# Performance work log

Hardware: AMD Instinct MI355X
Metric: run time of the kernel (lower is better)

Reference implementation:

```python
import jax, jax.numpy as jnp
import numpy as np

D = 128
N_NODES = 50000
N_EDGES = 500000


def layer_norm(x, g, b, eps=1e-5):
    m = jnp.mean(x, axis=-1, keepdims=True)
    v = jnp.var(x, axis=-1, keepdims=True)
    return (x - m) * jax.lax.rsqrt(v + eps) * g + b


def setup_inputs() -> dict:
    key = jax.random.key(0)
    ks = jax.random.split(key, 10)
    s = 1.0 / np.sqrt(D)  # torch Linear default-ish init scale
    return {
        "src": jax.random.normal(ks[0], (N_NODES, D), jnp.float32),
        "tgt": jax.random.normal(ks[1], (N_NODES, D), jnp.float32),
        "edge": jax.random.normal(ks[2], (N_EDGES, D), jnp.float32),
        "src_idx": jax.random.randint(ks[3], (N_EDGES,), 0, N_NODES, jnp.int64 if jax.config.jax_enable_x64 else jnp.int32),
        "tgt_idx": jax.random.randint(ks[4], (N_EDGES,), 0, N_NODES, jnp.int64 if jax.config.jax_enable_x64 else jnp.int32),
        "W_s2e": jax.random.normal(ks[5], (D, D), jnp.float32) * s,
        "W_t2e": jax.random.normal(ks[6], (D, D), jnp.float32) * s,
        "W_e2e": jax.random.normal(ks[7], (D, D), jnp.float32) * s,
        "W_e2t": jax.random.normal(ks[8], (D, D), jnp.float32) * s,
        "W_t2t": jax.random.normal(ks[9], (D, D), jnp.float32) * s,
        "ln1_g": jnp.ones((D,), jnp.float32),
        "ln1_b": jnp.zeros((D,), jnp.float32),
        "ln2_g": jnp.ones((D,), jnp.float32),
        "ln2_b": jnp.zeros((D,), jnp.float32),
    }


def reference(src, tgt, edge, src_idx, tgt_idx,
              W_s2e, W_t2e, W_e2e, W_e2t, W_t2t,
              ln1_g, ln1_b, ln2_g, ln2_b):
    # ---- STE2E: source/target/edge -> edge update ----
    # gather endpoint node features per edge [E, D]
    msg = (src[src_idx] @ W_s2e.T
           + tgt[tgt_idx] @ W_t2e.T
           + edge @ W_e2e.T)
    edge_out = edge + layer_norm(jax.nn.silu(msg), ln1_g, ln1_b)

    # ---- ET2T: aggregate edges to target nodes, update targets ----
    agg = jax.ops.segment_sum(edge_out, tgt_idx, num_segments=tgt.shape[0])  # [N, D]
    tgt_msg = agg @ W_e2t.T + tgt @ W_t2t.T
    tgt_out = tgt + layer_norm(jax.nn.silu(tgt_msg), ln2_g, ln2_b)

    return edge_out, tgt_out
```

## Files before the change

### kernel.cpp

```cpp
#include <hip/hip_runtime.h>
#include <hip/hip_bf16.h>

#define D 128
#define LDSPAD 136

typedef short s8v __attribute__((ext_vector_type(8)));
typedef float f4v __attribute__((ext_vector_type(4)));

__device__ inline short f2bf(float f) {
    __hip_bfloat16 h = __float2bfloat16(f);
    return *reinterpret_cast<short*>(&h);
}

__device__ inline void load_w_lds(const float* __restrict__ W, short* lds) {
    const int tid = threadIdx.x;
    const float4* W4 = reinterpret_cast<const float4*>(W);
#pragma unroll
    for (int i = 0; i < 16; ++i) {
        int f = tid + 256 * i;
        float4 v = W4[f];
        int row = f >> 5;
        int c4  = (f & 31) * 4;
        short* p = &lds[row * LDSPAD + c4];
        p[0] = f2bf(v.x); p[1] = f2bf(v.y);
        p[2] = f2bf(v.z); p[3] = f2bf(v.w);
    }
}

__device__ inline void mfma_tile(const float* __restrict__ X, int row0,
                                 const short* lds, f4v acc[8]) {
    const int lane = threadIdx.x & 63;
    const int l15 = lane & 15, q = lane >> 4;
    s8v a[4];
    const float* xr = X + (size_t)(row0 + l15) * D + q * 8;
#pragma unroll
    for (int c = 0; c < 4; ++c) {
        float4 f0 = *reinterpret_cast<const float4*>(xr + c * 32);
        float4 f1 = *reinterpret_cast<const float4*>(xr + c * 32 + 4);
        s8v t;
        t[0] = f2bf(f0.x); t[1] = f2bf(f0.y); t[2] = f2bf(f0.z); t[3] = f2bf(f0.w);
        t[4] = f2bf(f1.x); t[5] = f2bf(f1.y); t[6] = f2bf(f1.z); t[7] = f2bf(f1.w);
        a[c] = t;
    }
#pragma unroll
    for (int t = 0; t < 8; ++t) {
        f4v acc_t = {0.f, 0.f, 0.f, 0.f};
#pragma unroll
        for (int c = 0; c < 4; ++c) {
            const s8v b = *reinterpret_cast<const s8v*>(
                &lds[(t * 16 + l15) * LDSPAD + c * 32 + q * 8]);
            acc_t = __builtin_amdgcn_mfma_f32_16x16x32_bf16(a[c], b, acc_t, 0, 0, 0);
        }
        acc[t] = acc_t;
    }
}


__global__ __launch_bounds__(256) void k_zero_i(int* p, int n) {
    int i = blockIdx.x * 256 + threadIdx.x;
    if (i < n) p[i] = 0;
}

__global__ __launch_bounds__(256) void k_hist(const int* __restrict__ tidx,
                                              int* __restrict__ cnt, int E) {
    int i = blockIdx.x * 256 + threadIdx.x;
    if (i < E) atomicAdd(&cnt[tidx[i]], 1);
}

__global__ __launch_bounds__(1024) void k_scan(const int* __restrict__ cnt,
                                               int* __restrict__ off,
                                               int* __restrict__ cursor, int n) {
    __shared__ int part[1024];
    const int tid = threadIdx.x;
    const int chunk = (n + 1023) / 1024;
    const int lo = tid * chunk;
    const int hi = min(lo + chunk, n);
    int s = 0;
    for (int i = lo; i < hi; ++i) s += cnt[i];
    part[tid] = s;
    __syncthreads();
    for (int d = 1; d < 1024; d <<= 1) {
        int v = (tid >= d) ? part[tid - d] : 0;
        __syncthreads();
        part[tid] += v;
        __syncthreads();
    }
    int run = part[tid] - s;
    for (int i = lo; i < hi; ++i) {
        off[i] = run;
        cursor[i] = run;
        run += cnt[i];
    }
    if (tid == 0) off[n] = part[1023];
}

__global__ __launch_bounds__(256) void k_scatter(const int* __restrict__ tidx,
                                                 int* __restrict__ cursor,
                                                 int* __restrict__ elist, int E) {
    int i = blockIdx.x * 256 + threadIdx.x;
    if (i < E) {
        int p = atomicAdd(&cursor[tidx[i]], 1);
        elist[p] = i;
    }
}


__global__ __launch_bounds__(256) void k_node_gemm(const float* __restrict__ X,
                                                   const float* __restrict__ W,
                                                   float* __restrict__ P, int nrows) {
    __shared__ short lds[D * LDSPAD];
    load_w_lds(W, lds);
    __syncthreads();
    const int lane = threadIdx.x & 63, wave = threadIdx.x >> 6;
    const int l15 = lane & 15, q = lane >> 4;
    const int ntiles = nrows >> 4;
    for (int tile = blockIdx.x * 4 + wave; tile < ntiles; tile += gridDim.x * 4) {
        f4v acc[8];
        mfma_tile(X, tile * 16, lds, acc);
#pragma unroll
        for (int t = 0; t < 8; ++t) {
            int col = t * 16 + l15;
#pragma unroll
            for (int r = 0; r < 4; ++r)
                P[(size_t)(tile * 16 + q * 4 + r) * D + col] = acc[t][r];
        }
    }
}

__global__ __launch_bounds__(256) void k_edge(const float* __restrict__ edge,
                                              const int* __restrict__ sidx,
                                              const int* __restrict__ tidx,
                                              const float* __restrict__ W,
                                              const float* __restrict__ Ps,
                                              const float* __restrict__ Pt,
                                              const float* __restrict__ g1,
                                              const float* __restrict__ b1,
                                              float* __restrict__ eout, int E) {
    __shared__ short lds[D * LDSPAD];
    load_w_lds(W, lds);
    __syncthreads();
    const int lane = threadIdx.x & 63, wave = threadIdx.x >> 6;
    const int l15 = lane & 15, q = lane >> 4;
    const int ntiles = E >> 4;
    for (int tile = blockIdx.x * 4 + wave; tile < ntiles; tile += gridDim.x * 4) {
        const int e0 = tile * 16;
        f4v acc[8];
        mfma_tile(edge, e0, lds, acc);
        int si[4], ti[4];
#pragma unroll
        for (int r = 0; r < 4; ++r) {
            si[r] = sidx[e0 + q * 4 + r];
            ti[r] = tidx[e0 + q * 4 + r];
        }
        float h[8][4];
        float s1[4] = {0.f, 0.f, 0.f, 0.f}, s2[4] = {0.f, 0.f, 0.f, 0.f};
#pragma unroll
        for (int t = 0; t < 8; ++t) {
            int col = t * 16 + l15;
#pragma unroll
            for (int r = 0; r < 4; ++r) {
                float m = acc[t][r] + Ps[(size_t)si[r] * D + col]
                                    + Pt[(size_t)ti[r] * D + col];
                float hh = m / (1.f + __expf(-m));
                h[t][r] = hh;
                s1[r] += hh;
                s2[r] += hh * hh;
            }
        }
#pragma unroll
        for (int m = 1; m < 16; m <<= 1) {
#pragma unroll
            for (int r = 0; r < 4; ++r) {
                s1[r] += __shfl_xor(s1[r], m, 64);
                s2[r] += __shfl_xor(s2[r], m, 64);
            }
        }
        float mean[4], rstd[4];
#pragma unroll
        for (int r = 0; r < 4; ++r) {
            float mu = s1[r] * (1.f / 128.f);
            float var = s2[r] * (1.f / 128.f) - mu * mu;
            mean[r] = mu;
            rstd[r] = rsqrtf(var + 1e-5f);
        }
#pragma unroll
        for (int t = 0; t < 8; ++t) {
            int col = t * 16 + l15;
            float gg = g1[col], bb = b1[col];
#pragma unroll
            for (int r = 0; r < 4; ++r) {
                int rowg = e0 + q * 4 + r;
                float v = edge[(size_t)rowg * D + col]
                          + ((h[t][r] - mean[r]) * rstd[r] * gg + bb);
                eout[(size_t)rowg * D + col] = v;
            }
        }
    }
}

__global__ __launch_bounds__(256) void k_agg(const float* __restrict__ eout,
                                             const int* __restrict__ off,
                                             const int* __restrict__ elist,
                                             float* __restrict__ agg, int N) {
    const int node = blockIdx.x * 4 + (threadIdx.x >> 6);
    const int lane = threadIdx.x & 63;
    if (node >= N) return;
    const int lo = off[node], hi = off[node + 1];
    float ax = 0.f, ay = 0.f;
    for (int j = lo; j < hi; ++j) {
        int e = elist[j];
        float2 v = *reinterpret_cast<const float2*>(&eout[(size_t)e * D + 2 * lane]);
        ax += v.x; ay += v.y;
    }
    float2 o = {ax, ay};
    *reinterpret_cast<float2*>(&agg[(size_t)node * D + 2 * lane]) = o;
}

__global__ __launch_bounds__(256) void k_node_update(const float* __restrict__ aggIn,
                                                     const float* __restrict__ W,
                                                     const float* __restrict__ Ptt,
                                                     const float* __restrict__ tgt,
                                                     const float* __restrict__ g2,
                                                     const float* __restrict__ b2,
                                                     float* __restrict__ out, int N) {
    __shared__ short lds[D * LDSPAD];
    load_w_lds(W, lds);
    __syncthreads();
    const int lane = threadIdx.x & 63, wave = threadIdx.x >> 6;
    const int l15 = lane & 15, q = lane >> 4;
    const int ntiles = N >> 4;
    for (int tile = blockIdx.x * 4 + wave; tile < ntiles; tile += gridDim.x * 4) {
        const int n0 = tile * 16;
        f4v acc[8];
        mfma_tile(aggIn, n0, lds, acc);
        float h[8][4];
        float s1[4] = {0.f, 0.f, 0.f, 0.f}, s2[4] = {0.f, 0.f, 0.f, 0.f};
#pragma unroll
        for (int t = 0; t < 8; ++t) {
            int col = t * 16 + l15;
#pragma unroll
            for (int r = 0; r < 4; ++r) {
                int rowg = n0 + q * 4 + r;
                float m = acc[t][r] + Ptt[(size_t)rowg * D + col];
                float hh = m / (1.f + __expf(-m));
                h[t][r] = hh;
                s1[r] += hh;
                s2[r] += hh * hh;
            }
        }
#pragma unroll
        for (int m = 1; m < 16; m <<= 1) {
#pragma unroll
            for (int r = 0; r < 4; ++r) {
                s1[r] += __shfl_xor(s1[r], m, 64);
                s2[r] += __shfl_xor(s2[r], m, 64);
            }
        }
        float mean[4], rstd[4];
#pragma unroll
        for (int r = 0; r < 4; ++r) {
            float mu = s1[r] * (1.f / 128.f);
            float var = s2[r] * (1.f / 128.f) - mu * mu;
            mean[r] = mu;
            rstd[r] = rsqrtf(var + 1e-5f);
        }
#pragma unroll
        for (int t = 0; t < 8; ++t) {
            int col = t * 16 + l15;
            float gg = g2[col], bb = b2[col];
#pragma unroll
            for (int r = 0; r < 4; ++r) {
                int rowg = n0 + q * 4 + r;
                float v = tgt[(size_t)rowg * D + col]
                          + ((h[t][r] - mean[r]) * rstd[r] * gg + bb);
                out[(size_t)rowg * D + col] = v;
            }
        }
    }
}

extern "C" void kernel_launch(void* const* d_in, const int* in_sizes, int n_in,
                              void* d_out, int out_size, void* d_ws, size_t ws_size,
                              hipStream_t stream) {
    const float* src   = (const float*)d_in[0];
    const float* tgt   = (const float*)d_in[1];
    const float* edge  = (const float*)d_in[2];
    const int*   sidx  = (const int*)d_in[3];
    const int*   tidx  = (const int*)d_in[4];
    const float* W_s2e = (const float*)d_in[5];
    const float* W_t2e = (const float*)d_in[6];
    const float* W_e2e = (const float*)d_in[7];
    const float* W_e2t = (const float*)d_in[8];
    const float* W_t2t = (const float*)d_in[9];
    const float* g1    = (const float*)d_in[10];
    const float* b1    = (const float*)d_in[11];
    const float* g2    = (const float*)d_in[12];
    const float* b2    = (const float*)d_in[13];

    const int N = in_sizes[0] / D;
    const int E = in_sizes[3];

    float* eout = (float*)d_out;
    float* nout = eout + (size_t)E * D;

    float* Ps  = (float*)d_ws;
    float* Pt  = Ps + (size_t)N * D;
    float* Ptt = Pt + (size_t)N * D;
    int*   cnt    = (int*)(Ptt + (size_t)N * D);
    int*   off    = cnt + N;
    int*   cursor = off + N + 1;
    int*   elist  = cursor + N;

    k_zero_i<<<(N + 255) / 256, 256, 0, stream>>>(cnt, N);
    k_hist<<<(E + 255) / 256, 256, 0, stream>>>(tidx, cnt, E);
    k_scan<<<1, 1024, 0, stream>>>(cnt, off, cursor, N);
    k_scatter<<<(E + 255) / 256, 256, 0, stream>>>(tidx, cursor, elist, E);

    const int nodeBlocks = (N / 16 + 3) / 4;
    k_node_gemm<<<nodeBlocks, 256, 0, stream>>>(src, W_s2e, Ps, N);
    k_node_gemm<<<nodeBlocks, 256, 0, stream>>>(tgt, W_t2e, Pt, N);
    k_node_gemm<<<nodeBlocks, 256, 0, stream>>>(tgt, W_t2t, Ptt, N);

    k_edge<<<1024, 256, 0, stream>>>(edge, sidx, tidx, W_e2e, Ps, Pt, g1, b1,
                                     eout, E);

    k_agg<<<(N + 3) / 4, 256, 0, stream>>>(eout, off, elist, nout, N);
    k_node_update<<<nodeBlocks, 256, 0, stream>>>(nout, W_e2t, Ptt, tgt, g2, b2,
                                                  nout, N);
}
```

Before: 914.5 us.

## Preconvert weights to bf16 once, fuse tgt GEMMs, drop LDS in node kernels

A new prep kernel converts all five weight matrices to bf16 in workspace and also zeroes the histogram counts, replacing the separate zero kernel. The two GEMMs that read tgt are fused into one kernel so the A tile is built once. Node kernels now use one tile per wave and read B straight from global or L2 instead of staging it in LDS, and they declare occupancy hints. The edge kernel copies the pre-converted bf16 weights into LDS, uses a reciprocal-based SiLU, and is split into two launches over halves of the edges. These changes aim to cut repeated fp32-to-bf16 conversion, weight staging and extra reads of tgt, at the cost of more global B traffic and one extra launch.

```diff
diff --git a/kernel.cpp b/kernel.cpp
--- a/kernel.cpp
+++ b/kernel.cpp
@@ -5,6 +5,7 @@
 #define LDSPAD 136
 
 typedef short s8v __attribute__((ext_vector_type(8)));
+typedef short s4v __attribute__((ext_vector_type(4)));
 typedef float f4v __attribute__((ext_vector_type(4)));
 
 __device__ inline short f2bf(float f) {
@@ -12,26 +13,50 @@
     return *reinterpret_cast<short*>(&h);
 }
 
-__device__ inline void load_w_lds(const float* __restrict__ W, short* lds) {
+__device__ inline float fast_silu(float m) {
+    return m * __builtin_amdgcn_rcpf(1.f + __expf(-m));
+}
+
+__global__ __launch_bounds__(256) void k_prep(const float* __restrict__ W0,
+                                              const float* __restrict__ W1,
+                                              const float* __restrict__ W2,
+                                              const float* __restrict__ W3,
+                                              const float* __restrict__ W4,
+                                              short* __restrict__ Wbf,
+                                              int* __restrict__ cnt, int N) {
+    const int b = blockIdx.x, tid = threadIdx.x;
+    if (b < 80) {
+        int g = b * 256 + tid;
+        int m = g >> 12;
+        const float* W = W0;
+        if (m == 1) W = W1; else if (m == 2) W = W2;
+        else if (m == 3) W = W3; else if (m == 4) W = W4;
+        int w = g & 4095;
+        float4 v = reinterpret_cast<const float4*>(W)[w];
+        s4v o;
+        o[0] = f2bf(v.x); o[1] = f2bf(v.y); o[2] = f2bf(v.z); o[3] = f2bf(v.w);
+        *reinterpret_cast<s4v*>(&Wbf[(size_t)m * 16384 + w * 4]) = o;
+    } else {
+        int i = (b - 80) * 256 + tid;
+        if (i < N) cnt[i] = 0;
+    }
+}
+
+__device__ inline void load_wbf_lds(const short* __restrict__ Wb, short* lds) {
     const int tid = threadIdx.x;
-    const float4* W4 = reinterpret_cast<const float4*>(W);
-#pragma unroll
-    for (int i = 0; i < 16; ++i) {
+    const int4* src = reinterpret_cast<const int4*>(Wb);
+#pragma unroll
+    for (int i = 0; i < 8; ++i) {
         int f = tid + 256 * i;
-        float4 v = W4[f];
-        int row = f >> 5;
-        int c4  = (f & 31) * 4;
-        short* p = &lds[row * LDSPAD + c4];
-        p[0] = f2bf(v.x); p[1] = f2bf(v.y);
-        p[2] = f2bf(v.z); p[3] = f2bf(v.w);
-    }
-}
-
-__device__ inline void mfma_tile(const float* __restrict__ X, int row0,
-                                 const short* lds, f4v acc[8]) {
+        int4 v = src[f];
+        int row = f >> 4, c = f & 15;
+        *reinterpret_cast<int4*>(&lds[row * LDSPAD + c * 8]) = v;
+    }
+}
+
+__device__ inline void build_a(const float* __restrict__ X, int row0, s8v a[4]) {
     const int lane = threadIdx.x & 63;
     const int l15 = lane & 15, q = lane >> 4;
-    s8v a[4];
     const float* xr = X + (size_t)(row0 + l15) * D + q * 8;
 #pragma unroll
     for (int c = 0; c < 4; ++c) {
@@ -42,6 +67,11 @@
         t[4] = f2bf(f1.x); t[5] = f2bf(f1.y); t[6] = f2bf(f1.z); t[7] = f2bf(f1.w);
         a[c] = t;
     }
+}
+
+__device__ inline void mfma_b_lds(const s8v a[4], const short* lds, f4v acc[8]) {
+    const int lane = threadIdx.x & 63;
+    const int l15 = lane & 15, q = lane >> 4;
 #pragma unroll
     for (int t = 0; t < 8; ++t) {
         f4v acc_t = {0.f, 0.f, 0.f, 0.f};
@@ -55,11 +85,23 @@
     }
 }
 
-
-__global__ __launch_bounds__(256) void k_zero_i(int* p, int n) {
-    int i = blockIdx.x * 256 + threadIdx.x;
-    if (i < n) p[i] = 0;
-}
+__device__ inline void mfma_b_g(const s8v a[4], const short* __restrict__ Wb,
+                                f4v acc[8]) {
+    const int lane = threadIdx.x & 63;
+    const int l15 = lane & 15, q = lane >> 4;
+#pragma unroll
+    for (int t = 0; t < 8; ++t) {
+        f4v acc_t = {0.f, 0.f, 0.f, 0.f};
+#pragma unroll
+        for (int c = 0; c < 4; ++c) {
+            const s8v b = *reinterpret_cast<const s8v*>(
+                &Wb[(t * 16 + l15) * D + c * 32 + q * 8]);
+            acc_t = __builtin_amdgcn_mfma_f32_16x16x32_bf16(a[c], b, acc_t, 0, 0, 0);
+        }
+        acc[t] = acc_t;
+    }
+}
+
 
 __global__ __launch_bounds__(256) void k_hist(const int* __restrict__ tidx,
                                               int* __restrict__ cnt, int E) {
@@ -105,54 +147,80 @@
 }
 
 
-__global__ __launch_bounds__(256) void k_node_gemm(const float* __restrict__ X,
-                                                   const float* __restrict__ W,
-                                                   float* __restrict__ P, int nrows) {
+__global__ __launch_bounds__(256, 4) void k_gemm1(const float* __restrict__ X,
+                                                  const short* __restrict__ Wb,
+                                                  float* __restrict__ P, int ntiles) {
+    const int lane = threadIdx.x & 63, wave = threadIdx.x >> 6;
+    const int l15 = lane & 15, q = lane >> 4;
+    const int tile = blockIdx.x * 4 + wave;
+    if (tile >= ntiles) return;
+    s8v a[4];
+    build_a(X, tile * 16, a);
+    f4v acc[8];
+    mfma_b_g(a, Wb, acc);
+#pragma unroll
+    for (int t = 0; t < 8; ++t) {
+        int col = t * 16 + l15;
+#pragma unroll
+        for (int r = 0; r < 4; ++r)
+            P[(size_t)(tile * 16 + q * 4 + r) * D + col] = acc[t][r];
+    }
+}
+
+__global__ __launch_bounds__(256, 4) void k_gemm2(const float* __restrict__ X,
+                                                  const short* __restrict__ Wb1,
+                                                  const short* __restrict__ Wb2,
+                                                  float* __restrict__ P1,
+                                                  float* __restrict__ P2, int ntiles) {
+    const int lane = threadIdx.x & 63, wave = threadIdx.x >> 6;
+    const int l15 = lane & 15, q = lane >> 4;
+    const int tile = blockIdx.x * 4 + wave;
+    if (tile >= ntiles) return;
+    s8v a[4];
+    build_a(X, tile * 16, a);
+    f4v acc1[8], acc2[8];
+    mfma_b_g(a, Wb1, acc1);
+    mfma_b_g(a, Wb2, acc2);
+#pragma unroll
+    for (int t = 0; t < 8; ++t) {
+        int col = t * 16 + l15;
+#pragma unroll
+        for (int r = 0; r < 4; ++r) {
+            size_t o = (size_t)(tile * 16 + q * 4 + r) * D + col;
+            P1[o] = acc1[t][r];
+            P2[o] = acc2[t][r];
+        }
+    }
+}
+
+__global__ __launch_bounds__(256, 4) void k_edge(const float* __restrict__ edge,
+                                                 const int* __restrict__ sidx,
+                                                 const int* __restrict__ tidx,
+                                                 const short* __restrict__ Wb,
+                                                 const float* __restrict__ Ps,
+                                                 const float* __restrict__ Pt,
+                                                 const float* __restrict__ g1,
+                                                 const float* __restrict__ b1,
+                                                 float* __restrict__ eout,
+                                                 int tile0, int tile1) {
     __shared__ short lds[D * LDSPAD];
-    load_w_lds(W, lds);
+    load_wbf_lds(Wb, lds);
     __syncthreads();
     const int lane = threadIdx.x & 63, wave = threadIdx.x >> 6;
     const int l15 = lane & 15, q = lane >> 4;
-    const int ntiles = nrows >> 4;
-    for (int tile = blockIdx.x * 4 + wave; tile < ntiles; tile += gridDim.x * 4) {
-        f4v acc[8];
-        mfma_tile(X, tile * 16, lds, acc);
-#pragma unroll
-        for (int t = 0; t < 8; ++t) {
-            int col = t * 16 + l15;
-#pragma unroll
-            for (int r = 0; r < 4; ++r)
-                P[(size_t)(tile * 16 + q * 4 + r) * D + col] = acc[t][r];
-        }
-    }
-}
-
-__global__ __launch_bounds__(256) void k_edge(const float* __restrict__ edge,
-                                              const int* __restrict__ sidx,
-                                              const int* __restrict__ tidx,
-                                              const float* __restrict__ W,
-                                              const float* __restrict__ Ps,
-                                              const float* __restrict__ Pt,
-                                              const float* __restrict__ g1,
-                                              const float* __restrict__ b1,
-                                              float* __restrict__ eout, int E) {
-    __shared__ short lds[D * LDSPAD];
-    load_w_lds(W, lds);
-    __syncthreads();
-    const int lane = threadIdx.x & 63, wave = threadIdx.x >> 6;
-    const int l15 = lane & 15, q = lane >> 4;
-    const int ntiles = E >> 4;
-    for (int tile = blockIdx.x * 4 + wave; tile < ntiles; tile += gridDim.x * 4) {
+    for (int tile = tile0 + blockIdx.x * 4 + wave; tile < tile1;
+         tile += gridDim.x * 4) {
         const int e0 = tile * 16;
-        f4v acc[8];
-        mfma_tile(edge, e0, lds, acc);
         int si[4], ti[4];
 #pragma unroll
         for (int r = 0; r < 4; ++r) {
             si[r] = sidx[e0 + q * 4 + r];
             ti[r] = tidx[e0 + q * 4 + r];
         }
-        float h[8][4];
+        s8v a[4];
+        build_a(edge, e0, a);
+        f4v acc[8];
+        mfma_b_lds(a, lds, acc);
         float s1[4] = {0.f, 0.f, 0.f, 0.f}, s2[4] = {0.f, 0.f, 0.f, 0.f};
 #pragma unroll
         for (int t = 0; t < 8; ++t) {
@@ -161,8 +229,8 @@
             for (int r = 0; r < 4; ++r) {
                 float m = acc[t][r] + Ps[(size_t)si[r] * D + col]
                                     + Pt[(size_t)ti[r] * D + col];
-                float hh = m / (1.f + __expf(-m));
-                h[t][r] = hh;
+                float hh = fast_silu(m);
+                acc[t][r] = hh;
                 s1[r] += hh;
                 s2[r] += hh * hh;
             }
@@ -191,7 +259,7 @@
             for (int r = 0; r < 4; ++r) {
                 int rowg = e0 + q * 4 + r;
                 float v = edge[(size_t)rowg * D + col]
-                          + ((h[t][r] - mean[r]) * rstd[r] * gg + bb);
+                          + ((acc[t][r] - mean[r]) * rstd[r] * gg + bb);
                 eout[(size_t)rowg * D + col] = v;
             }
         }
@@ -216,65 +284,62 @@
     *reinterpret_cast<float2*>(&agg[(size_t)node * D + 2 * lane]) = o;
 }
 
-__global__ __launch_bounds__(256) void k_node_update(const float* __restrict__ aggIn,
-                                                     const float* __restrict__ W,
-                                                     const float* __restrict__ Ptt,
-                                                     const float* __restrict__ tgt,
-                                                     const float* __restrict__ g2,
-                                                     const float* __restrict__ b2,
-                                                     float* __restrict__ out, int N) {
-    __shared__ short lds[D * LDSPAD];
-    load_w_lds(W, lds);
-    __syncthreads();
+__global__ __launch_bounds__(256, 4) void k_node_update(const float* __restrict__ aggIn,
+                                                        const short* __restrict__ Wb,
+                                                        const float* __restrict__ Ptt,
+                                                        const float* __restrict__ tgt,
+                                                        const float* __restrict__ g2,
+                                                        const float* __restrict__ b2,
+                                                        float* __restrict__ out, int ntiles) {
     const int lane = threadIdx.x & 63, wave = threadIdx.x >> 6;
     const int l15 = lane & 15, q = lane >> 4;
-    const int ntiles = N >> 4;
-    for (int tile = blockIdx.x * 4 + wave; tile < ntiles; tile += gridDim.x * 4) {
-        const int n0 = tile * 16;
-        f4v acc[8];
-        mfma_tile(aggIn, n0, lds, acc);
-        float h[8][4];
-        float s1[4] = {0.f, 0.f, 0.f, 0.f}, s2[4] = {0.f, 0.f, 0.f, 0.f};
-#pragma unroll
-        for (int t = 0; t < 8; ++t) {
-            int col = t * 16 + l15;
-#pragma unroll
-            for (int r = 0; r < 4; ++r) {
-                int rowg = n0 + q * 4 + r;
-                float m = acc[t][r] + Ptt[(size_t)rowg * D + col];
-                float hh = m / (1.f + __expf(-m));
-                h[t][r] = hh;
-                s1[r] += hh;
-                s2[r] += hh * hh;
-            }
-        }
-#pragma unroll
-        for (int m = 1; m < 16; m <<= 1) {
-#pragma unroll
-            for (int r = 0; r < 4; ++r) {
-                s1[r] += __shfl_xor(s1[r], m, 64);
-                s2[r] += __shfl_xor(s2[r], m, 64);
-            }
-        }
-        float mean[4], rstd[4];
-#pragma unroll
-        for (int r = 0; r < 4; ++r) {
-            float mu = s1[r] * (1.f / 128.f);
-            float var = s2[r] * (1.f / 128.f) - mu * mu;
-            mean[r] = mu;
-            rstd[r] = rsqrtf(var + 1e-5f);
-        }
-#pragma unroll
-        for (int t = 0; t < 8; ++t) {
-            int col = t * 16 + l15;
-            float gg = g2[col], bb = b2[col];
-#pragma unroll
-            for (int r = 0; r < 4; ++r) {
-                int rowg = n0 + q * 4 + r;
-                float v = tgt[(size_t)rowg * D + col]
-                          + ((h[t][r] - mean[r]) * rstd[r] * gg + bb);
-                out[(size_t)rowg * D + col] = v;
-            }
+    const int tile = blockIdx.x * 4 + wave;
+    if (tile >= ntiles) return;
+    const int n0 = tile * 16;
+    s8v a[4];
+    build_a(aggIn, n0, a);
+    f4v acc[8];
+    mfma_b_g(a, Wb, acc);
+    float s1[4] = {0.f, 0.f, 0.f, 0.f}, s2[4] = {0.f, 0.f, 0.f, 0.f};
+#pragma unroll
+    for (int t = 0; t < 8; ++t) {
+        int col = t * 16 + l15;
+#pragma unroll
+        for (int r = 0; r < 4; ++r) {
+            int rowg = n0 + q * 4 + r;
+            float m = acc[t][r] + Ptt[(size_t)rowg * D + col];
+            float hh = fast_silu(m);
+            acc[t][r] = hh;
+            s1[r] += hh;
+            s2[r] += hh * hh;
+        }
+    }
+#pragma unroll
+    for (int m = 1; m < 16; m <<= 1) {
+#pragma unroll
+        for (int r = 0; r < 4; ++r) {
+            s1[r] += __shfl_xor(s1[r], m, 64);
+            s2[r] += __shfl_xor(s2[r], m, 64);
+        }
+    }
+    float mean[4], rstd[4];
+#pragma unroll
+    for (int r = 0; r < 4; ++r) {
+        float mu = s1[r] * (1.f / 128.f);
+        float var = s2[r] * (1.f / 128.f) - mu * mu;
+        mean[r] = mu;
+        rstd[r] = rsqrtf(var + 1e-5f);
+    }
+#pragma unroll
+    for (int t = 0; t < 8; ++t) {
+        int col = t * 16 + l15;
+        float gg = g2[col], bb = b2[col];
+#pragma unroll
+        for (int r = 0; r < 4; ++r) {
+            int rowg = n0 + q * 4 + r;
+            float v = tgt[(size_t)rowg * D + col]
+                      + ((acc[t][r] - mean[r]) * rstd[r] * gg + bb);
+            out[(size_t)rowg * D + col] = v;
         }
     }
 }
@@ -303,7 +368,8 @@
     float* eout = (float*)d_out;
     float* nout = eout + (size_t)E * D;
 
-    float* Ps  = (float*)d_ws;
+    short* Wbf = (short*)d_ws;
+    float* Ps  = (float*)(Wbf + 5 * 16384);
     float* Pt  = Ps + (size_t)N * D;
     float* Ptt = Pt + (size_t)N * D;
     int*   cnt    = (int*)(Ptt + (size_t)N * D);
@@ -311,20 +377,33 @@
     int*   cursor = off + N + 1;
     int*   elist  = cursor + N;
 
-    k_zero_i<<<(N + 255) / 256, 256, 0, stream>>>(cnt, N);
+    const short* Wb_s2e = Wbf;
+    const short* Wb_t2e = Wbf + 1 * 16384;
+    const short* Wb_e2e = Wbf + 2 * 16384;
+    const short* Wb_e2t = Wbf + 3 * 16384;
+    const short* Wb_t2t = Wbf + 4 * 16384;
+
+    const int zeroBlocks = (N + 255) / 256;
+    k_prep<<<80 + zeroBlocks, 256, 0, stream>>>(W_s2e, W_t2e, W_e2e, W_e2t, W_t2t,
+                                                Wbf, cnt, N);
+
     k_hist<<<(E + 255) / 256, 256, 0, stream>>>(tidx, cnt, E);
     k_scan<<<1, 1024, 0, stream>>>(cnt, off, cursor, N);
     k_scatter<<<(E + 255) / 256, 256, 0, stream>>>(tidx, cursor, elist, E);
 
-    const int nodeBlocks = (N / 16 + 3) / 4;
-    k_node_gemm<<<nodeBlocks, 256, 0, stream>>>(src, W_s2e, Ps, N);
-    k_node_gemm<<<nodeBlocks, 256, 0, stream>>>(tgt, W_t2e, Pt, N);
-    k_node_gemm<<<nodeBlocks, 256, 0, stream>>>(tgt, W_t2t, Ptt, N);
-
-    k_edge<<<1024, 256, 0, stream>>>(edge, sidx, tidx, W_e2e, Ps, Pt, g1, b1,
-                                     eout, E);
+    const int ntilesN = N >> 4;
+    const int nodeBlocks = (ntilesN + 3) / 4;
+    k_gemm1<<<nodeBlocks, 256, 0, stream>>>(src, Wb_s2e, Ps, ntilesN);
+    k_gemm2<<<nodeBlocks, 256, 0, stream>>>(tgt, Wb_t2e, Wb_t2t, Pt, Ptt, ntilesN);
+
+    const int ntilesE = E >> 4;
+    const int halfE = ntilesE >> 1;
+    k_edge<<<1024, 256, 0, stream>>>(edge, sidx, tidx, Wb_e2e, Ps, Pt, g1, b1,
+                                     eout, 0, halfE);
+    k_edge<<<1024, 256, 0, stream>>>(edge, sidx, tidx, Wb_e2e, Ps, Pt, g1, b1,
+                                     eout, halfE, ntilesE);
 
     k_agg<<<(N + 3) / 4, 256, 0, stream>>>(eout, off, elist, nout, N);
-    k_node_update<<<nodeBlocks, 256, 0, stream>>>(nout, W_e2t, Ptt, tgt, g2, b2,
-                                                  nout, N);
-}
+    k_node_update<<<nodeBlocks, 256, 0, stream>>>(nout, Wb_e2t, Ptt, tgt, g2, b2,
+                                                  nout, ntilesN);
+}
```

Result: slower. 1.199 ms (+31.2%).
